# Performance work log

Hardware: AMD Instinct MI355X
Metric: run time of the kernel (lower is better)

Reference implementation:

```python
import jax, jax.numpy as jnp
import numpy as np

D_MODEL = 1024
N_HEADS = 16
MIXTURE_FACTOR = 4
LATENT = D_MODEL // MIXTURE_FACTOR  # 256
D_K = D_MODEL // N_HEADS            # 64
B, L = 2, 2048


def setup_inputs() -> dict:
    key = jax.random.key(0)
    ks = jax.random.split(key, 13)
    s_in = 1.0 / np.sqrt(D_MODEL)
    s_lat = 1.0 / np.sqrt(LATENT)
    return {
        "queries": jax.random.normal(ks[0], (B, L, 1, D_MODEL), jnp.float32),
        "keys": jax.random.normal(ks[1], (B, L, 1, D_MODEL), jnp.float32),
        "values": jax.random.normal(ks[2], (B, L, 1, D_MODEL), jnp.float32),
        "Wq": jax.random.normal(ks[3], (D_MODEL, D_MODEL), jnp.float32) * s_in,
        "bq": jnp.zeros((D_MODEL,), jnp.float32),
        "Wd": jax.random.normal(ks[4], (D_MODEL, LATENT), jnp.float32) * s_in,
        "bd": jnp.zeros((LATENT,), jnp.float32),
        "Wk": jax.random.normal(ks[5], (LATENT, D_MODEL), jnp.float32) * s_lat,
        "bk": jnp.zeros((D_MODEL,), jnp.float32),
        "Wv": jax.random.normal(ks[6], (LATENT, D_MODEL), jnp.float32) * s_lat,
        "bv": jnp.zeros((D_MODEL,), jnp.float32),
        "Wo": jax.random.normal(ks[7], (D_MODEL, D_MODEL), jnp.float32) * s_in,
        "bo": jnp.zeros((D_MODEL,), jnp.float32),
    }


def reference(queries, keys, values, Wq, bq, Wd, bd, Wk, bk, Wv, bv, Wo, bo):
    b, l, h_in, e = queries.shape  # h_in == 1, e == d_model
    s = keys.shape[1]
    scale = D_K ** -0.5

    q_flat = queries.reshape(b, l, e)
    Q = (q_flat @ Wq + bq).reshape(b, l, N_HEADS, D_K)

    kv_input = keys.reshape(b, s, e)
    latent = kv_input @ Wd + bd                      # [b, s, latent]
    K = (latent @ Wk + bk).reshape(b, s, N_HEADS, D_K)
    V = (latent @ Wv + bv).reshape(b, s, N_HEADS, D_K)

    scores = jnp.einsum('blhe,bshe->bhls', Q, K) * scale  # [b, h, l, s]
    causal = jnp.triu(jnp.ones((l, s), dtype=bool), k=1)
    scores = jnp.where(causal, -jnp.inf, scores)
    A = jax.nn.softmax(scores, axis=-1)

    out = jnp.einsum('bhls,bshd->blhd', A, V).reshape(b, l, N_HEADS * D_K)
    return out @ Wo + bo
```

## Files before the change

kernel.cpp:

```cpp
#include <hip/hip_runtime.h>
#include <stdint.h>


#define DM 1024
#define NH 16
#define DK 64
#define LL 2048

typedef float  f32x4  __attribute__((ext_vector_type(4)));
typedef __bf16 bf16x8 __attribute__((ext_vector_type(8)));
typedef short  s16x8  __attribute__((ext_vector_type(8)));

__device__ __forceinline__ unsigned short f2bf(float f) {
    union { float f; unsigned int u; } v; v.f = f;
    return (unsigned short)((v.u + 0x7fffu + ((v.u >> 16) & 1u)) >> 16);
}
__device__ __forceinline__ unsigned int pack2(float a, float b) {
    return (unsigned int)f2bf(a) | ((unsigned int)f2bf(b) << 16);
}
__device__ __forceinline__ bf16x8 ld8(const unsigned short* p) {
    s16x8 s = *(const s16x8*)p;
    return __builtin_bit_cast(bf16x8, s);
}
__device__ __forceinline__ void gl16(const void* g, void* l) {
    __builtin_amdgcn_global_load_lds((__attribute__((address_space(1))) void*)(g),
                                     (__attribute__((address_space(3))) void*)(l),
                                     16, 0, 0);
}

__global__ __launch_bounds__(256)
void prep_k(const float* __restrict__ Wq, const float* __restrict__ Wd,
            const float* __restrict__ Wk, const float* __restrict__ Wv,
            const float* __restrict__ Wo, const float* __restrict__ queries,
            const float* __restrict__ keys,
            unsigned short* __restrict__ WqT, unsigned short* __restrict__ WdT,
            unsigned short* __restrict__ WkvT, unsigned short* __restrict__ WoT,
            unsigned short* __restrict__ Qb, unsigned short* __restrict__ Kb) {
    int bid = blockIdx.x;
    const int t = threadIdx.x;

    const float* W; unsigned short* WT; int TK, TN;
    if (bid < 1024)      { W = Wq; WT = WqT;  TK = 1024; TN = 1024; }
    else if (bid < 1280) { bid -= 1024; W = Wd; WT = WdT; TK = 1024; TN = 256; }
    else if (bid < 1536) { bid -= 1280; W = Wk; WT = WkvT; TK = 256; TN = 1024; }
    else if (bid < 1792) { bid -= 1536; W = Wv; WT = WkvT + (size_t)1024 * 256; TK = 256; TN = 1024; }
    else if (bid < 2816) { bid -= 1792; W = Wo; WT = WoT;  TK = 1024; TN = 1024; }
    else {
        bid -= 2816;
        const float* src; unsigned short* dst;
        if (bid < 1024) { src = queries; dst = Qb; }
        else            { bid -= 1024; src = keys; dst = Kb; }
        const size_t base = (size_t)bid * 4096;
#pragma unroll
        for (int i = 0; i < 4; ++i) {
            float4 f = *(const float4*)(src + base + (size_t)(i * 256 + t) * 4);
            uint2 u = { pack2(f.x, f.y), pack2(f.z, f.w) };
            *(uint2*)(dst + base + (size_t)(i * 256 + t) * 4) = u;
        }
        return;
    }
    __shared__ float tile[32][33];
    const int tx = t & 31, ty = t >> 5;
    const int bx = bid % (TK / 32), by = bid / (TK / 32);
    const int k0 = bx * 32, n0 = by * 32;
#pragma unroll
    for (int i = 0; i < 4; ++i)
        tile[ty + 8 * i][tx] = W[(size_t)(k0 + ty + 8 * i) * TN + n0 + tx];
    __syncthreads();
#pragma unroll
    for (int i = 0; i < 4; ++i)
        WT[(size_t)(n0 + ty + 8 * i) * TK + k0 + tx] = f2bf(tile[tx][ty + 8 * i]);
}

template<int MODE>
__global__ __launch_bounds__(256)
void gemm64_k(const unsigned short* __restrict__ Ap, const unsigned short* __restrict__ Bt,
              const float* __restrict__ bias, void* __restrict__ Cp,
              const unsigned short* __restrict__ Ap2, const unsigned short* __restrict__ Bt2,
              const float* __restrict__ bias2, void* __restrict__ Cp2,
              int K) {
    __shared__ unsigned short As[64 * 64];
    __shared__ unsigned short Bs[64 * 64];

    int bid = blockIdx.x;
    const unsigned short* A;
    const unsigned short* B;
    const float* bs;
    bool second = false;
    int m0, n0;
    if (MODE == 2 && bid >= 1024) {
        bid -= 1024; A = Ap2; B = Bt2; bs = bias2; second = true;
        const int xcd = bid & 7, s = bid >> 3;
        n0 = (s & 3) * 64; m0 = (xcd * 8 + (s >> 2)) * 64;
    } else {
        A = Ap; B = Bt; bs = bias;
        const int xcd = bid & 7, s = bid >> 3;
        if (MODE == 3) { n0 = (s & 31) * 64; m0 = (xcd * 8 + (s >> 5)) * 64; }
        else           { n0 = (s & 15) * 64; m0 = (xcd * 8 + (s >> 4)) * 64; }
    }

    const int t = threadIdx.x, lane = t & 63, wv = t >> 6;
    const int quad = lane >> 4, l15 = lane & 15;

    const int lr8 = lane >> 3;
    const int g8 = (lane & 7) ^ (lr8 & 7);
    const unsigned short* gA = A + (size_t)(m0 + wv * 16 + lr8) * K + g8 * 8;
    const unsigned short* gB = B + (size_t)(n0 + wv * 16 + lr8) * K + g8 * 8;
    unsigned short* lA = As + wv * 1024;
    unsigned short* lB = Bs + wv * 1024;

    int aoff[2][2], boff[2][2];
#pragma unroll
    for (int i = 0; i < 2; ++i) {
        const int ra = (wv >> 1) * 32 + i * 16 + l15;
        const int rb = (wv & 1) * 32 + i * 16 + l15;
#pragma unroll
        for (int ks = 0; ks < 2; ++ks) {
            aoff[i][ks] = ra * 64 + (((ks * 4 + quad) ^ (ra & 7)) << 3);
            boff[i][ks] = rb * 64 + (((ks * 4 + quad) ^ (rb & 7)) << 3);
        }
    }

    f32x4 acc[2][2] = {};
    for (int kk = 0; kk < K; kk += 64) {
        __syncthreads();
        gl16(gA + kk, lA);               gl16(gA + kk + (size_t)8 * K, lA + 512);
        gl16(gB + kk, lB);               gl16(gB + kk + (size_t)8 * K, lB + 512);
        __syncthreads();
#pragma unroll
        for (int ks = 0; ks < 2; ++ks) {
            bf16x8 a[2], b[2];
#pragma unroll
            for (int i = 0; i < 2; ++i) a[i] = ld8(As + aoff[i][ks]);
#pragma unroll
            for (int j = 0; j < 2; ++j) b[j] = ld8(Bs + boff[j][ks]);
#pragma unroll
            for (int i = 0; i < 2; ++i)
#pragma unroll
                for (int j = 0; j < 2; ++j)
                    acc[i][j] = __builtin_amdgcn_mfma_f32_16x16x32_bf16(a[i], b[j], acc[i][j], 0, 0, 0);
        }
    }

#pragma unroll
    for (int j = 0; j < 2; ++j) {
        const int col = n0 + (wv & 1) * 32 + j * 16 + l15;
        const bool isV = (MODE == 3) && (col >= 1024);
        const float bvv = isV ? bias2[col - 1024] : bs[col];
#pragma unroll
        for (int i = 0; i < 2; ++i) {
            const int rowb = m0 + (wv >> 1) * 32 + i * 16 + quad * 4;
#pragma unroll
            for (int r = 0; r < 4; ++r) {
                const float v = acc[i][j][r] + bvv;
                const int row = rowb + r;
                if (MODE == 1)
                    ((float*)Cp)[(size_t)row * 1024 + col] = v;
                else if (MODE == 2) {
                    if (second) ((unsigned short*)Cp2)[(size_t)row * 256 + col] = f2bf(v);
                    else        ((unsigned short*)Cp)[(size_t)row * 1024 + col] = f2bf(v);
                } else {
                    if (!isV)   ((unsigned short*)Cp)[(size_t)row * 1024 + col] = f2bf(v);
                    else        ((unsigned short*)Cp2)[((size_t)(row >> 11) * 1024 + (col - 1024)) * LL
                                                       + (row & (LL - 1))] = f2bf(v);
                }
            }
        }
    }
}

__global__ __launch_bounds__(512)
void attn5_k(const unsigned short* __restrict__ Qp,
             const unsigned short* __restrict__ Kp,
             const unsigned short* __restrict__ VpT,
             unsigned short* __restrict__ Op) {
    __shared__ unsigned short Ks[2][4096];
    __shared__ unsigned short Vs[2][4096];
    __shared__ unsigned short Ps[8][16][72];

    const int t = threadIdx.x, lane = t & 63, wv = t >> 6;
    const int grp = wv >> 2, w4 = wv & 3;
    const int quad = lane >> 4, l15 = lane & 15;

    const int bid = blockIdx.x;
    const int xcd = bid & 7, s = bid >> 3;
    const int pair = s & 15;
    const int combo = xcd * 4 + (s >> 4);
    const int h = combo & 15, b = combo >> 4;

    const int srow = w4 * 16 + (lane >> 3);
    const int g8 = (lane & 7) ^ ((lane >> 3) & 7);
    unsigned short* lK = &Ks[grp][w4 * 1024];
    unsigned short* lV = &Vs[grp][w4 * 1024];
    const int sw = l15 & 7;
    float* cb = (float*)&Ks[0][0];

    for (int tsel = 0; tsel < 2; ++tsel) {
        const int tile = tsel ? (31 - pair) : pair;
        const int q0 = tile * 64;

        const unsigned short* qp = Qp + (size_t)(b * LL + q0 + w4 * 16 + l15) * DM + h * DK;
        const bf16x8 aq0 = ld8(qp + quad * 8);
        const bf16x8 aq1 = ld8(qp + 32 + quad * 8);

        f32x4 acc[4] = {};
        float lrow[4] = {0.f, 0.f, 0.f, 0.f};
        const int rowq = q0 + w4 * 16 + quad * 4;

        const int nit = tile / 2 + 1;
        for (int it = 0; it < nit; ++it) {
            const int c = 2 * it + grp;
            const bool active = (c <= tile);
            const int kt = c * 64;
            __syncthreads();
            if (active) {
                const unsigned short* kg = Kp + (size_t)(b * LL + kt + srow) * DM + h * DK + g8 * 8;
                const unsigned short* vg = VpT + ((size_t)(b * NH + h) * DK + srow) * LL + kt + g8 * 8;
                gl16(kg, lK);             gl16(kg + (size_t)8 * DM, lK + 512);
                gl16(vg, lV);             gl16(vg + (size_t)8 * LL, lV + 512);
            }
            __syncthreads();
            if (!active) continue;

            f32x4 s4[4];
#pragma unroll
            for (int sub = 0; sub < 4; ++sub) {
                const int base = (sub * 16 + l15) * 64;
                f32x4 ss = {};
                bf16x8 b0 = ld8(&Ks[grp][base + ((quad ^ sw) << 3)]);
                ss = __builtin_amdgcn_mfma_f32_16x16x32_bf16(aq0, b0, ss, 0, 0, 0);
                bf16x8 b1 = ld8(&Ks[grp][base + (((4 + quad) ^ sw) << 3)]);
                ss = __builtin_amdgcn_mfma_f32_16x16x32_bf16(aq1, b1, ss, 0, 0, 0);
                s4[sub] = ss;
            }

            const bool diag = (c == tile);
#pragma unroll
            for (int sub = 0; sub < 4; ++sub) {
                const int col = kt + sub * 16 + l15;
#pragma unroll
                for (int r = 0; r < 4; ++r) {
                    float e = exp2f(fmaf(s4[sub][r], 0.18033688011112042f, -16.0f));
                    if (diag && col > rowq + r) e = 0.f;
                    lrow[r] += e;
                    Ps[wv][quad * 4 + r][sub * 16 + l15] =
                        (unsigned short)(__builtin_bit_cast(unsigned int, e) >> 16);
                }
            }

#pragma unroll
            for (int ks = 0; ks < 2; ++ks) {
                bf16x8 ap = ld8(&Ps[wv][l15][ks * 32 + quad * 8]);
#pragma unroll
                for (int sub = 0; sub < 4; ++sub) {
                    bf16x8 bv = ld8(&Vs[grp][(sub * 16 + l15) * 64 + (((ks * 4 + quad) ^ sw) << 3)]);
                    acc[sub] = __builtin_amdgcn_mfma_f32_16x16x32_bf16(ap, bv, acc[sub], 0, 0, 0);
                }
            }
        }

        __syncthreads();
        const int base = (w4 * 64 + lane) * 20;
        if (grp == 1) {
#pragma unroll
            for (int sub = 0; sub < 4; ++sub)
#pragma unroll
                for (int r = 0; r < 4; ++r) cb[base + sub * 4 + r] = acc[sub][r];
#pragma unroll
            for (int r = 0; r < 4; ++r) cb[base + 16 + r] = lrow[r];
        }
        __syncthreads();
        if (grp == 0) {
#pragma unroll
            for (int sub = 0; sub < 4; ++sub)
#pragma unroll
                for (int r = 0; r < 4; ++r) acc[sub][r] += cb[base + sub * 4 + r];
#pragma unroll
            for (int r = 0; r < 4; ++r) {
                lrow[r] += cb[base + 16 + r];
#pragma unroll
                for (int off = 1; off < 16; off <<= 1)
                    lrow[r] += __shfl_xor(lrow[r], off, 64);
                lrow[r] = __builtin_amdgcn_rcpf(lrow[r]);
            }
#pragma unroll
            for (int sub = 0; sub < 4; ++sub)
#pragma unroll
                for (int r = 0; r < 4; ++r)
                    Op[(size_t)(b * LL + rowq + r) * DM + h * DK + sub * 16 + l15] =
                        f2bf(acc[sub][r] * lrow[r]);
        }
    }
}

extern "C" void kernel_launch(void* const* d_in, const int* in_sizes, int n_in,
                              void* d_out, int out_size, void* d_ws, size_t ws_size,
                              hipStream_t stream) {
    const float* queries = (const float*)d_in[0];
    const float* keys    = (const float*)d_in[1];
    const float* Wq = (const float*)d_in[3];  const float* bq = (const float*)d_in[4];
    const float* Wd = (const float*)d_in[5];  const float* bd = (const float*)d_in[6];
    const float* Wk = (const float*)d_in[7];  const float* bk = (const float*)d_in[8];
    const float* Wv = (const float*)d_in[9];  const float* bv = (const float*)d_in[10];
    const float* Wo = (const float*)d_in[11]; const float* bo = (const float*)d_in[12];

    char* ws = (char*)d_ws;
    const size_t MB = 1048576;
    unsigned short* Qp   = (unsigned short*)(ws);
    unsigned short* Kb   = (unsigned short*)(ws + 8 * MB);
    unsigned short* Kp   = (unsigned short*)(ws + 8 * MB);
    unsigned short* Qb   = (unsigned short*)(ws + 16 * MB);
    unsigned short* VpT  = (unsigned short*)(ws + 16 * MB);
    unsigned short* WqT  = (unsigned short*)(ws + 24 * MB);
    unsigned short* Lat  = (unsigned short*)(ws + 26 * MB);
    unsigned short* WdT  = (unsigned short*)(ws + 28 * MB);
    unsigned short* WkvT = (unsigned short*)(ws + 28 * MB + 524288);
    unsigned short* Attn = (unsigned short*)(ws + 24 * MB);
    unsigned short* WoT  = (unsigned short*)(ws + 32 * MB);

    prep_k<<<4864, 256, 0, stream>>>(Wq, Wd, Wk, Wv, Wo, queries, keys,
                                     WqT, WdT, WkvT, WoT, Qb, Kb);
    gemm64_k<2><<<1280, 256, 0, stream>>>(Qb, WqT, bq, Qp, Kb, WdT, bd, Lat, 1024);
    gemm64_k<3><<<2048, 256, 0, stream>>>(Lat, WkvT, bk, Kp, nullptr, nullptr, bv, VpT, 256);
    attn5_k<<<512, 512, 0, stream>>>(Qp, Kp, VpT, Attn);
    gemm64_k<1><<<1024, 256, 0, stream>>>(Attn, WoT, bo, d_out, nullptr, nullptr, nullptr, nullptr, 1024);
}
```

Measured before the change: 209.4 us.

## Enlarge GEMM tiles to 128x64, stage V transpose through LDS, split diagonal softmax path

All projection GEMMs move from 64x64 to 128x64 output tiles, so each wave computes 4x2 MFMA fragments. This halves the grid sizes and raises operand reuse per LDS load. The transposed V output is now written through a shared-memory staging buffer with 16-byte coalesced stores instead of scattered 2-byte stores. The attention kernel also separates the diagonal tile from off-diagonal tiles, so the causal mask compare is skipped on most tiles. The trade-off is more registers and LDS per block and fewer blocks, which may reduce occupancy and tail balance.

```diff
diff --git a/kernel.cpp b/kernel.cpp
--- a/kernel.cpp
+++ b/kernel.cpp
@@ -74,13 +74,14 @@
 
 template<int MODE>
 __global__ __launch_bounds__(256)
-void gemm64_k(const unsigned short* __restrict__ Ap, const unsigned short* __restrict__ Bt,
-              const float* __restrict__ bias, void* __restrict__ Cp,
-              const unsigned short* __restrict__ Ap2, const unsigned short* __restrict__ Bt2,
-              const float* __restrict__ bias2, void* __restrict__ Cp2,
-              int K) {
-    __shared__ unsigned short As[64 * 64];
-    __shared__ unsigned short Bs[64 * 64];
+void gemm_k(const unsigned short* __restrict__ Ap, const unsigned short* __restrict__ Bt,
+            const float* __restrict__ bias, void* __restrict__ Cp,
+            const unsigned short* __restrict__ Ap2, const unsigned short* __restrict__ Bt2,
+            const float* __restrict__ bias2, void* __restrict__ Cp2,
+            int K) {
+    __shared__ unsigned short Sh[12288];
+    unsigned short* As = Sh;
+    unsigned short* Bs = Sh + 8192;
 
     int bid = blockIdx.x;
     const unsigned short* A;
@@ -88,15 +89,15 @@
     const float* bs;
     bool second = false;
     int m0, n0;
-    if (MODE == 2 && bid >= 1024) {
-        bid -= 1024; A = Ap2; B = Bt2; bs = bias2; second = true;
+    if (MODE == 0 && bid >= 512) {
+        bid -= 512; A = Ap2; B = Bt2; bs = bias2; second = true;
         const int xcd = bid & 7, s = bid >> 3;
-        n0 = (s & 3) * 64; m0 = (xcd * 8 + (s >> 2)) * 64;
+        n0 = (s & 3) * 64; m0 = (xcd * 4 + (s >> 2)) * 128;
     } else {
         A = Ap; B = Bt; bs = bias;
         const int xcd = bid & 7, s = bid >> 3;
-        if (MODE == 3) { n0 = (s & 31) * 64; m0 = (xcd * 8 + (s >> 5)) * 64; }
-        else           { n0 = (s & 15) * 64; m0 = (xcd * 8 + (s >> 4)) * 64; }
+        if (MODE == 2) { n0 = (s & 31) * 64; m0 = (xcd * 4 + (s >> 5)) * 128; }
+        else           { n0 = (s & 15) * 64; m0 = (xcd * 4 + (s >> 4)) * 128; }
     }
 
     const int t = threadIdx.x, lane = t & 63, wv = t >> 6;
@@ -104,73 +105,105 @@
 
     const int lr8 = lane >> 3;
     const int g8 = (lane & 7) ^ (lr8 & 7);
-    const unsigned short* gA = A + (size_t)(m0 + wv * 16 + lr8) * K + g8 * 8;
+    const unsigned short* gA = A + (size_t)(m0 + wv * 32 + lr8) * K + g8 * 8;
     const unsigned short* gB = B + (size_t)(n0 + wv * 16 + lr8) * K + g8 * 8;
-    unsigned short* lA = As + wv * 1024;
+    unsigned short* lA = As + wv * 2048;
     unsigned short* lB = Bs + wv * 1024;
 
-    int aoff[2][2], boff[2][2];
-#pragma unroll
-    for (int i = 0; i < 2; ++i) {
-        const int ra = (wv >> 1) * 32 + i * 16 + l15;
-        const int rb = (wv & 1) * 32 + i * 16 + l15;
+    int aoff[4][2], boff[2][2];
+#pragma unroll
+    for (int i = 0; i < 4; ++i) {
+        const int ra = (wv >> 1) * 64 + i * 16 + l15;
+#pragma unroll
+        for (int ks = 0; ks < 2; ++ks)
+            aoff[i][ks] = ra * 64 + (((ks * 4 + quad) ^ (ra & 7)) << 3);
+    }
+#pragma unroll
+    for (int j = 0; j < 2; ++j) {
+        const int rb = (wv & 1) * 32 + j * 16 + l15;
+#pragma unroll
+        for (int ks = 0; ks < 2; ++ks)
+            boff[j][ks] = rb * 64 + (((ks * 4 + quad) ^ (rb & 7)) << 3);
+    }
+
+    f32x4 acc[4][2] = {};
+    for (int kk = 0; kk < K; kk += 64) {
+        __syncthreads();
+#pragma unroll
+        for (int s = 0; s < 4; ++s) gl16(gA + kk + (size_t)s * 8 * K, lA + s * 512);
+#pragma unroll
+        for (int s = 0; s < 2; ++s) gl16(gB + kk + (size_t)s * 8 * K, lB + s * 512);
+        __syncthreads();
 #pragma unroll
         for (int ks = 0; ks < 2; ++ks) {
-            aoff[i][ks] = ra * 64 + (((ks * 4 + quad) ^ (ra & 7)) << 3);
-            boff[i][ks] = rb * 64 + (((ks * 4 + quad) ^ (rb & 7)) << 3);
-        }
-    }
-
-    f32x4 acc[2][2] = {};
-    for (int kk = 0; kk < K; kk += 64) {
-        __syncthreads();
-        gl16(gA + kk, lA);               gl16(gA + kk + (size_t)8 * K, lA + 512);
-        gl16(gB + kk, lB);               gl16(gB + kk + (size_t)8 * K, lB + 512);
-        __syncthreads();
-#pragma unroll
-        for (int ks = 0; ks < 2; ++ks) {
-            bf16x8 a[2], b[2];
-#pragma unroll
-            for (int i = 0; i < 2; ++i) a[i] = ld8(As + aoff[i][ks]);
+            bf16x8 a[4], b[2];
+#pragma unroll
+            for (int i = 0; i < 4; ++i) a[i] = ld8(As + aoff[i][ks]);
 #pragma unroll
             for (int j = 0; j < 2; ++j) b[j] = ld8(Bs + boff[j][ks]);
 #pragma unroll
-            for (int i = 0; i < 2; ++i)
+            for (int i = 0; i < 4; ++i)
 #pragma unroll
                 for (int j = 0; j < 2; ++j)
                     acc[i][j] = __builtin_amdgcn_mfma_f32_16x16x32_bf16(a[i], b[j], acc[i][j], 0, 0, 0);
         }
     }
 
-#pragma unroll
-    for (int j = 0; j < 2; ++j) {
-        const int col = n0 + (wv & 1) * 32 + j * 16 + l15;
-        const bool isV = (MODE == 3) && (col >= 1024);
-        const float bvv = isV ? bias2[col - 1024] : bs[col];
-#pragma unroll
-        for (int i = 0; i < 2; ++i) {
-            const int rowb = m0 + (wv >> 1) * 32 + i * 16 + quad * 4;
-#pragma unroll
-            for (int r = 0; r < 4; ++r) {
-                const float v = acc[i][j][r] + bvv;
-                const int row = rowb + r;
-                if (MODE == 1)
-                    ((float*)Cp)[(size_t)row * 1024 + col] = v;
-                else if (MODE == 2) {
-                    if (second) ((unsigned short*)Cp2)[(size_t)row * 256 + col] = f2bf(v);
-                    else        ((unsigned short*)Cp)[(size_t)row * 1024 + col] = f2bf(v);
-                } else {
-                    if (!isV)   ((unsigned short*)Cp)[(size_t)row * 1024 + col] = f2bf(v);
-                    else        ((unsigned short*)Cp2)[((size_t)(row >> 11) * 1024 + (col - 1024)) * LL
-                                                       + (row & (LL - 1))] = f2bf(v);
+    const bool isV = (MODE == 2) && (n0 >= 1024);
+    if (!isV) {
+#pragma unroll
+        for (int j = 0; j < 2; ++j) {
+            const int col = n0 + (wv & 1) * 32 + j * 16 + l15;
+            const float bvv = bs[col];
+            const int cstride = second ? 256 : 1024;
+#pragma unroll
+            for (int i = 0; i < 2; ++i) {}
+#pragma unroll
+            for (int i = 0; i < 4; ++i) {
+                const int rowb = m0 + (wv >> 1) * 64 + i * 16 + quad * 4;
+#pragma unroll
+                for (int r = 0; r < 4; ++r) {
+                    const float v = acc[i][j][r] + bvv;
+                    const int row = rowb + r;
+                    if (MODE == 1)
+                        ((float*)Cp)[(size_t)row * 1024 + col] = v;
+                    else if (second)
+                        ((unsigned short*)Cp2)[(size_t)row * 256 + col] = f2bf(v);
+                    else
+                        ((unsigned short*)Cp)[(size_t)row * 1024 + col] = f2bf(v);
                 }
             }
         }
+    } else {
+        __syncthreads();
+        unsigned short* Ld = Sh;
+#pragma unroll
+        for (int j = 0; j < 2; ++j) {
+            const int dloc = (wv & 1) * 32 + j * 16 + l15;
+            const float bvv = bias2[(n0 - 1024) + dloc];
+#pragma unroll
+            for (int i = 0; i < 4; ++i) {
+                const int tokb = (wv >> 1) * 64 + i * 16 + quad * 4;
+#pragma unroll
+                for (int r = 0; r < 4; ++r)
+                    Ld[dloc * 136 + tokb + r] = f2bf(acc[i][j][r] + bvv);
+            }
+        }
+        __syncthreads();
+        const int dloc = t >> 2;
+        const int tk0 = (t & 3) * 32;
+        const int bb = m0 >> 11;
+        unsigned short* dst = (unsigned short*)Cp2 +
+            ((size_t)bb * 1024 + (n0 - 1024) + dloc) * LL + (m0 & (LL - 1)) + tk0;
+        const unsigned short* srcp = Ld + dloc * 136 + tk0;
+#pragma unroll
+        for (int c = 0; c < 4; ++c)
+            *(uint4*)(dst + c * 8) = *(const uint4*)(srcp + c * 8);
     }
 }
 
 __global__ __launch_bounds__(512)
-void attn5_k(const unsigned short* __restrict__ Qp,
+void attn6_k(const unsigned short* __restrict__ Qp,
              const unsigned short* __restrict__ Kp,
              const unsigned short* __restrict__ VpT,
              unsigned short* __restrict__ Op) {
@@ -234,17 +267,29 @@
                 s4[sub] = ss;
             }
 
-            const bool diag = (c == tile);
-#pragma unroll
-            for (int sub = 0; sub < 4; ++sub) {
-                const int col = kt + sub * 16 + l15;
-#pragma unroll
-                for (int r = 0; r < 4; ++r) {
-                    float e = exp2f(fmaf(s4[sub][r], 0.18033688011112042f, -16.0f));
-                    if (diag && col > rowq + r) e = 0.f;
-                    lrow[r] += e;
-                    Ps[wv][quad * 4 + r][sub * 16 + l15] =
-                        (unsigned short)(__builtin_bit_cast(unsigned int, e) >> 16);
+            if (c == tile) {
+#pragma unroll
+                for (int sub = 0; sub < 4; ++sub) {
+                    const int col = kt + sub * 16 + l15;
+#pragma unroll
+                    for (int r = 0; r < 4; ++r) {
+                        float e = exp2f(fmaf(s4[sub][r], 0.18033688011112042f, -16.0f));
+                        if (col > rowq + r) e = 0.f;
+                        lrow[r] += e;
+                        Ps[wv][quad * 4 + r][sub * 16 + l15] =
+                            (unsigned short)(__builtin_bit_cast(unsigned int, e) >> 16);
+                    }
+                }
+            } else {
+#pragma unroll
+                for (int sub = 0; sub < 4; ++sub) {
+#pragma unroll
+                    for (int r = 0; r < 4; ++r) {
+                        float e = exp2f(fmaf(s4[sub][r], 0.18033688011112042f, -16.0f));
+                        lrow[r] += e;
+                        Ps[wv][quad * 4 + r][sub * 16 + l15] =
+                            (unsigned short)(__builtin_bit_cast(unsigned int, e) >> 16);
+                    }
                 }
             }
 
@@ -320,8 +365,8 @@
 
     prep_k<<<4864, 256, 0, stream>>>(Wq, Wd, Wk, Wv, Wo, queries, keys,
                                      WqT, WdT, WkvT, WoT, Qb, Kb);
-    gemm64_k<2><<<1280, 256, 0, stream>>>(Qb, WqT, bq, Qp, Kb, WdT, bd, Lat, 1024);
-    gemm64_k<3><<<2048, 256, 0, stream>>>(Lat, WkvT, bk, Kp, nullptr, nullptr, bv, VpT, 256);
-    attn5_k<<<512, 512, 0, stream>>>(Qp, Kp, VpT, Attn);
-    gemm64_k<1><<<1024, 256, 0, stream>>>(Attn, WoT, bo, d_out, nullptr, nullptr, nullptr, nullptr, 1024);
-}
+    gemm_k<0><<<640, 256, 0, stream>>>(Qb, WqT, bq, Qp, Kb, WdT, bd, Lat, 1024);
+    gemm_k<2><<<1024, 256, 0, stream>>>(Lat, WkvT, bk, Kp, nullptr, nullptr, bv, VpT, 256);
+    attn6_k<<<512, 512, 0, stream>>>(Qp, Kp, VpT, Attn);
+    gemm_k<1><<<512, 256, 0, stream>>>(Attn, WoT, bo, d_out, nullptr, nullptr, nullptr, nullptr, 1024);
+}
```

New measurement: 205.5 us. About the same (-1.9%).
